# Kernel optimization log

Hardware: AMD Instinct MI355X
Metric: run time of the kernel (lower is better)

The kernel has to match this reference:

```python
import jax, jax.numpy as jnp
from jax import lax
import numpy as np

B = 128   # per-stream batch (hard-coded via torch.zeros(128, ...))
T = 224   # timesteps
L = 224   # per-timestep signal length
H = 12    # LSTM hidden size


def _conv_chain(x, w1, b1, w2, b2):
    # x: [N, 1, 224] -> [N, 1, 28]
    # Conv1d(k=8, s=4, p=2) -> ReLU -> MaxPool1d(k=4, s=2, p=1) -> ReLU -> Conv1d(k=3, s=1, p=1) -> ReLU
    y = lax.conv_general_dilated(x, w1, (4,), [(2, 2)]) + b1[None, :, None]          # [N,1,56]
    y = jax.nn.relu(y)
    y = lax.reduce_window(y, -jnp.inf, lax.max, (1, 1, 4), (1, 1, 2),
                          [(0, 0), (0, 0), (1, 1)])                                   # [N,1,28]
    y = jax.nn.relu(y)
    y = lax.conv_general_dilated(y, w2, (1,), [(1, 1)]) + b2[None, :, None]          # [N,1,28]
    return jax.nn.relu(y)


def _lstm_bidir(x, Wih, Whh, b):
    # x: [B, T, D]; Wih: [2, 4H, D]; Whh: [2, 4H, H]; b: [2, 4H]; gates in PyTorch order i,f,g,o
    Bn, hid = x.shape[0], Whh.shape[-1]

    def run(xs, wih, whh, bb):
        def step(carry, xt):
            h, c = carry
            g = xt @ wih.T + h @ whh.T + bb
            i, f, gg, o = jnp.split(g, 4, axis=-1)
            c = jax.nn.sigmoid(f) * c + jax.nn.sigmoid(i) * jnp.tanh(gg)
            h = jax.nn.sigmoid(o) * jnp.tanh(c)
            return (h, c), h
        h0 = jnp.zeros((Bn, hid), x.dtype)
        _, ys = lax.scan(step, (h0, h0), xs)
        return ys

    xs = jnp.swapaxes(x, 0, 1)                     # [T, B, D]
    fwd = run(xs, Wih[0], Whh[0], b[0])
    bwd = run(xs[::-1], Whh_fix := Wih[1], Whh[1], b[1])[::-1]
    return jnp.swapaxes(jnp.concatenate([fwd, bwd], axis=-1), 0, 1)  # [B, T, 2H]


def _forward(x, c1w1, c1b1, c1w2, c1b2, c2w1, c2b1, c2w2, c2b2,
             l1_0_Wih, l1_0_Whh, l1_0_b, l1_1_Wih, l1_1_Whh, l1_1_b,
             l2_0_Wih, l2_0_Whh, l2_0_b, l2_1_Wih, l2_1_Whh, l2_1_b,
             fcw1, fcb1, fcw2, fcb2, fcw3, fcb3, w1, w2):
    x1 = x[:B, 0]          # [B, 224, 224]
    x2 = x[B:2 * B, 0]     # [B, 224, 224]
    # Fuse the 224-step Python loop: fold time into the batch of the 1D conv.
    y1 = _conv_chain(x1.reshape(B * T, 1, L), c1w1, c1b1, c1w2, c1b2).reshape(B, T, 28)
    y2 = _conv_chain(x2.reshape(B * T, 1, L), c2w1, c2b1, c2w2, c2b2).reshape(B, T, 28)
    o1 = _lstm_bidir(_lstm_bidir(y1, l1_0_Wih, l1_0_Whh, l1_0_b), l1_1_Wih, l1_1_Whh, l1_1_b)
    o2 = _lstm_bidir(_lstm_bidir(y2, l2_0_Wih, l2_0_Whh, l2_0_b), l2_1_Wih, l2_1_Whh, l2_1_b)
    out = w1 * o1 + w2 * o2                       # [B, T, 24]
    out = out.reshape(B, T * 2 * H)               # [B, 5376]
    out = out @ fcw1.T + fcb1                     # [B, 1024]
    out = out @ fcw2.T + fcb2                     # [B, 192]
    return out @ fcw3.T + fcb3                    # [B, 9]


def setup_inputs():
    key = jax.random.key(0)
    ks = iter(jax.random.split(key, 48))

    def rn(shape, scale=0.1):
        return (scale * jax.random.normal(next(ks), shape)).astype(jnp.float32)

    inp = {"x": rn((2 * B, 1, T, L), 1.0)}
    for s in ("c1", "c2"):
        inp[s + "w1"] = rn((1, 1, 8))
        inp[s + "b1"] = rn((1,))
        inp[s + "w2"] = rn((1, 1, 3))
        inp[s + "b2"] = rn((1,))
    for s in ("l1", "l2"):
        for layer, din in ((0, 28), (1, 2 * H)):
            inp[f"{s}_{layer}_Wih"] = rn((2, 4 * H, din))
            inp[f"{s}_{layer}_Whh"] = rn((2, 4 * H, H))
            inp[f"{s}_{layer}_b"] = rn((2, 4 * H))
    inp["fcw1"] = rn((1024, T * 2 * H), 0.02)
    inp["fcb1"] = rn((1024,))
    inp["fcw2"] = rn((192, 1024), 0.05)
    inp["fcb2"] = rn((192,))
    inp["fcw3"] = rn((9, 192), 0.05)
    inp["fcb3"] = rn((9,))
    inp["w1"] = jnp.ones((1,), jnp.float32)
    inp["w2"] = jnp.ones((1,), jnp.float32)
    return inp


def reference(x, c1w1, c1b1, c1w2, c1b2, c2w1, c2b1, c2w2, c2b2,
              l1_0_Wih, l1_0_Whh, l1_0_b, l1_1_Wih, l1_1_Whh, l1_1_b,
              l2_0_Wih, l2_0_Whh, l2_0_b, l2_1_Wih, l2_1_Whh, l2_1_b,
              fcw1, fcb1, fcw2, fcb2, fcw3, fcb3, w1, w2):
    return _forward(x, c1w1, c1b1, c1w2, c1b2, c2w1, c2b1, c2w2, c2b2,
                    l1_0_Wih, l1_0_Whh, l1_0_b, l1_1_Wih, l1_1_Whh, l1_1_b,
                    l2_0_Wih, l2_0_Whh, l2_0_b, l2_1_Wih, l2_1_Whh, l2_1_b,
                    fcw1, fcb1, fcw2, fcb2, fcw3, fcb3, w1, w2)
```

## Files before the change

kernel.cpp:

```cpp
#include <hip/hip_runtime.h>

#define BB 128
#define TT 224
#define LL 224

typedef float v2f __attribute__((ext_vector_type(2)));

__device__ __forceinline__ float rcpf(float x){ return __builtin_amdgcn_rcpf(x); }

#if __has_builtin(__builtin_amdgcn_exp2f)
#define EXP2(x) __builtin_amdgcn_exp2f(x)
#else
#define EXP2(x) __expf((x)*0.6931471805599453f)
#endif

template<int N>
__device__ __forceinline__ float rorN(float x){
  int xi = __builtin_bit_cast(int, x);
  xi = __builtin_amdgcn_update_dpp(xi, xi, 0x120 + N, 0xf, 0xf, false);
  return __builtin_bit_cast(float, xi);
}

__device__ __forceinline__ void swap32(float& a, float& b){
  asm volatile("s_nop 1\n\tv_permlane32_swap_b32 %0, %1\n\ts_nop 1"
               : "+v"(a), "+v"(b));
}

__global__ __launch_bounds__(256) void convpre_kernel(const float* __restrict__ x,
    const float* __restrict__ c1w1, const float* __restrict__ c1b1,
    const float* __restrict__ c1w2, const float* __restrict__ c1b2,
    const float* __restrict__ c2w1, const float* __restrict__ c2b1,
    const float* __restrict__ c2w2, const float* __restrict__ c2b2,
    const float* __restrict__ l10Wih, const float* __restrict__ l10b,
    const float* __restrict__ l20Wih, const float* __restrict__ l20b,
    float* __restrict__ pre,
    const float* __restrict__ fcw2, const float* __restrict__ fcw3,
    float* __restrict__ Wtb)
{
  __shared__ float sb[1440];
  int gb  = blockIdx.x;
  int tid = threadIdx.x;

  if (gb < 36){
    int idx = gb*256 + tid;
    int o = idx >> 10, n = idx & 1023;
    float acc = 0.f;
    for (int p=0;p<192;p++) acc += fcw3[o*192+p]*fcw2[(size_t)p*1024+n];
    Wtb[idx] = acc;
    return;
  }

  float* c1s  = sb;
  float* y4   = sb + 912;

  int blk = gb - 36;
  int branch = (blk >= 1792);
  int lblk = blk - branch*1792;
  int b  = lblk / 14;
  int t0 = (lblk - b*14)*16;
  size_t rbase = ((size_t)(branch*128 + b))*224 + t0;
  size_t prow  = (size_t)b*224 + t0;

  const float* w1 = branch ? c2w1 : c1w1;
  const float* w2 = branch ? c2w2 : c1w2;
  float b1  = branch ? c2b1[0] : c1b1[0];
  float b2v = branch ? c2b2[0] : c1b2[0];
  const float* wih = branch ? l20Wih : l10Wih;
  const float* bia = branch ? l20b   : l10b;

  if (tid < 224){
    int row  = tid / 14, quad = tid - row*14;
    int cj0  = quad*4;
    int bx   = 4*cj0 - 4;
    const float* xrow = x + (rbase + row)*224;
    float w1r[8];
    #pragma unroll
    for (int kk=0;kk<8;kk++) w1r[kk]=w1[kk];
    float xr[24];
    #pragma unroll
    for (int q=0;q<6;q++){
      int idx = bx + 4*q;
      if (idx >= 0 && idx <= 220){
        float4 v = *(const float4*)(xrow + idx);
        xr[4*q]=v.x; xr[4*q+1]=v.y; xr[4*q+2]=v.z; xr[4*q+3]=v.w;
      } else {
        #pragma unroll
        for (int e=0;e<4;e++){
          int ii = idx+e;
          xr[4*q+e] = (ii>=0 && ii<224) ? xrow[ii] : 0.f;
        }
      }
    }
    #pragma unroll
    for (int e=0;e<4;e++){
      float s = b1;
      #pragma unroll
      for (int kk=0;kk<8;kk++) s += xr[4*e+2+kk]*w1r[kk];
      c1s[row*57 + cj0 + e] = fmaxf(s, 0.f);
    }
  }
  __syncthreads();

  for (int i = tid; i < 448; i += 256){
    int row = i / 28, j = i - row*28;
    const float* cr = &c1s[row*57];
    float o = b2v;
    #pragma unroll
    for (int pi=0;pi<3;pi++){
      int p = j - 1 + pi;
      float pool = 0.f;
      if (p>=0 && p<28){
        int i0 = 2*p - 1;
        float m = -1e30f;
        #pragma unroll
        for (int q=0;q<4;q++){
          int ii = i0+q;
          if (ii>=0 && ii<56) m = fmaxf(m, cr[ii]);
        }
        pool = fmaxf(m, 0.f);
      }
      o += pool * w2[pi];
    }
    y4[row*32 + j] = fmaxf(o, 0.f);
  }
  __syncthreads();

  if (tid < 192){
    int d   = tid / 96;
    int g96 = tid - d*96;
    int row = g96 % 48;
    int rrg = g96 / 48;
    const float4* wr = (const float4*)(wih + (d*48 + row)*28);
    float4 wv[7];
    #pragma unroll
    for (int q=0;q<7;q++) wv[q] = wr[q];
    float bias = bia[d*48 + row];
    int unit = row % 12, g = row / 12;
    float* prebase = pre + (size_t)(2*branch + d)*(TT*BB*48) + unit*4 + g;
    #pragma unroll
    for (int rq=0; rq<8; rq++){
      int rr = rrg*8 + rq;
      const float4* yv = (const float4*)&y4[rr*32];
      float acc = bias;
      #pragma unroll
      for (int q=0;q<7;q++){
        float4 yq = yv[q];
        acc += yq.x*wv[q].x + yq.y*wv[q].y + yq.z*wv[q].z + yq.w*wv[q].w;
      }
      prebase[(prow + rr)*48] = acc;
    }
  }
}

#define LSTM_STEP(P, SS) { \
  float x1=rorN<1>(hv), x2=rorN<2>(hv), x3=rorN<3>(hv), x4=rorN<4>(hv), \
        x5=rorN<5>(hv), x6=rorN<6>(hv), x7=rorN<7>(hv), x8=rorN<8>(hv), \
        x9=rorN<9>(hv), x10=rorN<10>(hv), x11=rorN<11>(hv), x12=rorN<12>(hv), \
        x13=rorN<13>(hv), x14=rorN<14>(hv), x15=rorN<15>(hv); \
  v2f a0 = (P); \
  a0 += w[0]*(v2f){hv,hv};   a0 += w[1]*(v2f){x1,x1};   a0 += w[2]*(v2f){x2,x2};   a0 += w[3]*(v2f){x3,x3}; \
  v2f a1 = w[4]*(v2f){x4,x4};   a1 += w[5]*(v2f){x5,x5};   a1 += w[6]*(v2f){x6,x6};   a1 += w[7]*(v2f){x7,x7}; \
  v2f a2 = w[8]*(v2f){x8,x8};   a2 += w[9]*(v2f){x9,x9};   a2 += w[10]*(v2f){x10,x10}; a2 += w[11]*(v2f){x11,x11}; \
  v2f a3 = w[12]*(v2f){x12,x12}; a3 += w[13]*(v2f){x13,x13}; a3 += w[14]*(v2f){x14,x14}; a3 += w[15]*(v2f){x15,x15}; \
  v2f gg = (a0+a1)+(a2+a3); \
  v2f m  = gg*kmul; \
  v2f e  = { EXP2(m.x), EXP2(m.y) }; \
  e += (v2f){1.f,1.f}; \
  v2f d  = { rcpf(e.x), rcpf(e.y) }; \
  v2f res = ca*d + cb; \
  float p0 = res.x, p1 = res.x; swap32(p0, p1); \
  float q0 = res.y, q1 = res.y; swap32(q0, q1); \
  cst = fmaf(q0, cst, p0*p1); \
  float et = EXP2(cst*2.885390082f); \
  float dt = rcpf(et+1.f); \
  hv = q1*fmaf(-2.f, dt, 1.f); \
  hbuf[SS] = hv; }

#define FLUSH8 { \
  if (doSt){ \
    _Pragma("unroll") \
    for (int q=0;q<8;q++) outP[q*ostep] = hbuf[q]; \
  } \
  outP += 8*ostep; }

__global__ __launch_bounds__(64) __attribute__((amdgpu_waves_per_eu(1,1)))
void lstm_kernel(const float* __restrict__ pre,
    const float* __restrict__ whhA, const float* __restrict__ whhB,
    float* __restrict__ out,
    const float* __restrict__ fcw1, const float* __restrict__ fcb1,
    const float* __restrict__ Wtb,
    float* __restrict__ wpart, float* __restrict__ BCpart)
{
  __shared__ float wt[576];
  int blk  = blockIdx.x;
  int lane = threadIdx.x;

  if (blk >= 256){
    int xb  = blk - 256;
    int s   = xb / 84;
    int j64 = xb % 84;
    #pragma unroll
    for (int q=0;q<9;q++) wt[q*64+lane] = Wtb[q*1024 + s*64 + lane];
    __syncthreads();
    int j = j64*64 + lane;
    int nbase = s*64;
    float acc[9];
    #pragma unroll
    for (int o=0;o<9;o++) acc[o]=0.f;
    #pragma unroll 4
    for (int n4=0;n4<16;n4++){
      int nb = nbase + n4*4;
      float4 v4;
      v4.x = fcw1[(size_t)(nb  )*5376 + j];
      v4.y = fcw1[(size_t)(nb+1)*5376 + j];
      v4.z = fcw1[(size_t)(nb+2)*5376 + j];
      v4.w = fcw1[(size_t)(nb+3)*5376 + j];
      #pragma unroll
      for (int o=0;o<9;o++){
        float4 w4 = *(const float4*)&wt[o*64 + n4*4];
        acc[o] += v4.x*w4.x + v4.y*w4.y + v4.z*w4.z + v4.w*w4.w;
      }
    }
    #pragma unroll
    for (int o=0;o<9;o++) wpart[((size_t)s*9+o)*5376 + j] = acc[o];
    if (j64 == 0 && lane < 9){
      float bcp = 0.f;
      for (int n=0;n<64;n++) bcp += wt[lane*64+n]*fcb1[nbase+n];
      BCpart[s*9+lane] = bcp;
    }
    return;
  }

  int r    = blk >> 6;
  int br   = r >> 1, dir = r & 1;
  int u    = lane & 15;
  int bh   = (lane >> 4) & 1;
  int rbit = lane >> 5;
  int keff = (u < 12) ? u : 11;
  int b    = (blk & 63)*2 + bh;
  const float* whh = (br ? whhB : whhA) + dir*48*12;

  v2f w[16];
  #pragma unroll
  for (int rr=0; rr<16; rr++){
    int j = (u - rr) & 15;
    bool vld = (j < 12) && (u < 12);
    int uw = (u < 12) ? u : 0;
    int jw = (j < 12) ? j : 0;
    float wa = whh[((rbit?24:0)  + uw)*12 + jw];
    float wb = whh[((rbit?36:12) + uw)*12 + jw];
    w[rr] = (v2f){ vld ? wa : 0.f, vld ? wb : 0.f };
  }
  const v2f kmul = rbit ? (v2f){2.885390082f, -1.442695041f}
                        : (v2f){-1.442695041f, -1.442695041f};
  const v2f ca   = rbit ? (v2f){-2.f, 1.f} : (v2f){1.f, 1.f};
  const v2f cb   = rbit ? (v2f){ 1.f, 0.f} : (v2f){0.f, 0.f};

  const float* preR = pre + (size_t)r*(TT*BB*48) + (size_t)b*(TT*48) + keff*4 + rbit*2;
  const int sstep = dir ? -48 : 48;
  int scb = dir ? 223*48 : 0;

  v2f pcur[8], pnext[8];
  #pragma unroll
  for (int i=0;i<8;i++) pcur[i]  = *(const v2f*)(preR + scb +  i   *sstep);
  #pragma unroll
  for (int i=0;i<8;i++) pnext[i] = *(const v2f*)(preR + scb + (i+8)*sstep);
  int lb = scb + 16*sstep;

  float hv = 0.f, cst = 0.f;
  float hbuf[8];
  const int ostep = dir ? -24 : 24;
  float* outP = out + (size_t)br*(BB*TT*24) + (size_t)b*TT*24 + dir*12 + u
              + (size_t)(dir ? 223 : 0)*24;
  const bool doSt = (rbit==0) && (u < 12);

  for (int c=0;c<14;c++){
    LSTM_STEP(pcur[0],0) LSTM_STEP(pcur[1],1) LSTM_STEP(pcur[2],2) LSTM_STEP(pcur[3],3)
    LSTM_STEP(pcur[4],4) LSTM_STEP(pcur[5],5) LSTM_STEP(pcur[6],6) LSTM_STEP(pcur[7],7)
    FLUSH8
    if (c < 13){
      #pragma unroll
      for (int i=0;i<8;i++) pcur[i] = *(const v2f*)(preR + lb + i*sstep);
      lb += 8*sstep;
    }
    LSTM_STEP(pnext[0],0) LSTM_STEP(pnext[1],1) LSTM_STEP(pnext[2],2) LSTM_STEP(pnext[3],3)
    LSTM_STEP(pnext[4],4) LSTM_STEP(pnext[5],5) LSTM_STEP(pnext[6],6) LSTM_STEP(pnext[7],7)
    FLUSH8
    if (c < 13){
      #pragma unroll
      for (int i=0;i<8;i++) pnext[i] = *(const v2f*)(preR + lb + i*sstep);
      lb += 8*sstep;
    }
  }
}

__global__ __launch_bounds__(256) void pregate2_kernel(
    const float* __restrict__ in,
    const float* __restrict__ wihA, const float* __restrict__ biasA,
    const float* __restrict__ wihB, const float* __restrict__ biasB,
    float* __restrict__ pre,
    const float* __restrict__ wpart, float* __restrict__ Wc,
    const float* __restrict__ fcw3, const float* __restrict__ fcb2,
    const float* __restrict__ fcb3, const float* __restrict__ BCpart,
    float* __restrict__ BC)
{
  const int D = 24;
  __shared__ float sb[48*24 + 48];
  int gb  = blockIdx.x;
  int tid = threadIdx.x;

  if (gb < 189){
    int idx = gb*256 + tid;
    float a = 0.f;
    #pragma unroll
    for (int s=0;s<16;s++) a += wpart[(size_t)s*48384 + idx];
    Wc[idx] = a;
    return;
  }
  if (gb == 189){
    if (tid < 9){
      float acc = fcb3[tid];
      const float* f3 = fcw3 + tid*192;
      for (int p=0;p<192;p++) acc += f3[p]*fcb2[p];
      #pragma unroll
      for (int s=0;s<16;s++) acc += BCpart[s*9+tid];
      BC[tid] = acc;
    }
    return;
  }

  int pgb = gb - 190;
  float* wL = sb;
  float* bL = sb + 48*D;
  int r = pgb / 1344;
  int lin = (pgb % 1344)*256 + tid;
  int br = r>>1, dir = r&1;
  const float* wih  = (br ? wihB  : wihA)  + dir*48*D;
  const float* bias = (br ? biasB : biasA) + dir*48;
  for (int i = tid; i < 48*D; i += 256) wL[i]=wih[i];
  if (tid < 48) bL[tid]=bias[tid];
  __syncthreads();
  int tb = lin/12;  int k = lin - tb*12;
  const float* rowp = in + (size_t)br*688128 + (size_t)tb*D;
  float aI=bL[k], aF=bL[12+k], aG=bL[24+k], aO=bL[36+k];
  const float4* rp4 = (const float4*)rowp;
  #pragma unroll
  for (int d4=0; d4<D/4; d4++){
    float4 xv = rp4[d4];
    float4 wI = *(const float4*)&wL[(0*12+k)*D + d4*4];
    float4 wF = *(const float4*)&wL[(1*12+k)*D + d4*4];
    float4 wG = *(const float4*)&wL[(2*12+k)*D + d4*4];
    float4 wO = *(const float4*)&wL[(3*12+k)*D + d4*4];
    aI += xv.x*wI.x + xv.y*wI.y + xv.z*wI.z + xv.w*wI.w;
    aF += xv.x*wF.x + xv.y*wF.y + xv.z*wF.z + xv.w*wF.w;
    aG += xv.x*wG.x + xv.y*wG.y + xv.z*wG.z + xv.w*wG.w;
    aO += xv.x*wO.x + xv.y*wO.y + xv.z*wO.z + xv.w*wO.w;
  }
  float4* o = (float4*)(pre + (size_t)r*(TT*BB*48) + (size_t)tb*48 + k*4);
  *o = make_float4(aI,aF,aG,aO);
}

__global__ void final_kernel(const float* __restrict__ o1, const float* __restrict__ o2,
    const float* __restrict__ Wc, const float* __restrict__ BC,
    const float* __restrict__ w1p, const float* __restrict__ w2p,
    float* __restrict__ out)
{
  int wid  = blockIdx.x*4 + (threadIdx.x>>6);
  int lane = threadIdx.x & 63;
  if (wid >= 128*9) return;
  int m = wid / 9, o = wid - m*9;
  float w1 = w1p[0], w2 = w2p[0];
  const float* r1 = o1 + (size_t)m*5376;
  const float* r2 = o2 + (size_t)m*5376;
  const float* wc = Wc + (size_t)o*5376;
  float acc = 0.f;
  for (int i=lane;i<5376;i+=64){
    acc += (w1*r1[i] + w2*r2[i]) * wc[i];
  }
  #pragma unroll
  for (int off=32;off;off>>=1) acc += __shfl_down(acc, off);
  if (lane==0) out[m*9+o] = acc + BC[o];
}

extern "C" void kernel_launch(void* const* d_in, const int* in_sizes, int n_in,
                              void* d_out, int out_size, void* d_ws, size_t ws_size,
                              hipStream_t stream) {
  (void)in_sizes; (void)n_in; (void)out_size; (void)ws_size;
  const float* x    = (const float*)d_in[0];
  const float* c1w1 = (const float*)d_in[1];
  const float* c1b1 = (const float*)d_in[2];
  const float* c1w2 = (const float*)d_in[3];
  const float* c1b2 = (const float*)d_in[4];
  const float* c2w1 = (const float*)d_in[5];
  const float* c2b1 = (const float*)d_in[6];
  const float* c2w2 = (const float*)d_in[7];
  const float* c2b2 = (const float*)d_in[8];
  const float* l10Wih = (const float*)d_in[9];
  const float* l10Whh = (const float*)d_in[10];
  const float* l10b   = (const float*)d_in[11];
  const float* l11Wih = (const float*)d_in[12];
  const float* l11Whh = (const float*)d_in[13];
  const float* l11b   = (const float*)d_in[14];
  const float* l20Wih = (const float*)d_in[15];
  const float* l20Whh = (const float*)d_in[16];
  const float* l20b   = (const float*)d_in[17];
  const float* l21Wih = (const float*)d_in[18];
  const float* l21Whh = (const float*)d_in[19];
  const float* l21b   = (const float*)d_in[20];
  const float* fcw1 = (const float*)d_in[21];
  const float* fcb1 = (const float*)d_in[22];
  const float* fcw2 = (const float*)d_in[23];
  const float* fcb2 = (const float*)d_in[24];
  const float* fcw3 = (const float*)d_in[25];
  const float* fcb3 = (const float*)d_in[26];
  const float* w1   = (const float*)d_in[27];
  const float* w2   = (const float*)d_in[28];
  float* out = (float*)d_out;

  float* ws  = (float*)d_ws;
  float* wpart = ws;
  float* pre  = ws  + 2*802816;
  float* ol0  = pre + 4*1376256;
  float* ol1  = ol0 + 2*688128;
  float* Wc   = ol1 + 2*688128;
  float* BC   = Wc  + 48384;
  float* BCpart = BC + 9;
  float* Wtb  = BCpart + 144;

  convpre_kernel<<<3620,256,0,stream>>>(x, c1w1,c1b1,c1w2,c1b2, c2w1,c2b1,c2w2,c2b2,
      l10Wih, l10b, l20Wih, l20b, pre, fcw2, fcw3, Wtb);
  lstm_kernel<<<1600,64,0,stream>>>(pre, l10Whh, l20Whh, ol0,
      fcw1, fcb1, Wtb, wpart, BCpart);
  pregate2_kernel<<<5566,256,0,stream>>>(ol0, l11Wih, l11b, l21Wih, l21b, pre, wpart, Wc,
      fcw3, fcb2, fcb3, BCpart, BC);
  lstm_kernel<<<256,64,0,stream>>>(pre, l11Whh, l21Whh, ol1,
      fcw1, fcb1, Wtb, wpart, BCpart);
  final_kernel<<<288,256,0,stream>>>(ol1, ol1+688128, Wc, BC, w1, w2, out);
}
```

Measured before the change: 163.0 us.

## Move Wc/BC reduction into second LSTM launch and enlarge conv tiles

The Wc partial-sum reduction and BC bias computation move out of pregate2_kernel into spare blocks of the second lstm_kernel launch, selected by a phase flag. They now run alongside the latency-bound recurrent blocks, which otherwise leave the GPU mostly idle, and pregate2 sheds 190 blocks. convpre_kernel also handles 32 timesteps per block instead of 16, with 8 conv outputs per thread, halving the block count and amortizing weight loads at the cost of more shared memory and registers.

```diff
diff --git a/kernel.cpp b/kernel.cpp
--- a/kernel.cpp
+++ b/kernel.cpp
@@ -37,7 +37,7 @@
     const float* __restrict__ fcw2, const float* __restrict__ fcw3,
     float* __restrict__ Wtb)
 {
-  __shared__ float sb[1440];
+  __shared__ float sb[2848];
   int gb  = blockIdx.x;
   int tid = threadIdx.x;
 
@@ -51,13 +51,13 @@
   }
 
   float* c1s  = sb;
-  float* y4   = sb + 912;
+  float* y4   = sb + 1824;
 
   int blk = gb - 36;
-  int branch = (blk >= 1792);
-  int lblk = blk - branch*1792;
-  int b  = lblk / 14;
-  int t0 = (lblk - b*14)*16;
+  int branch = (blk >= 896);
+  int lblk = blk - branch*896;
+  int b  = lblk / 7;
+  int t0 = (lblk - b*7)*32;
   size_t rbase = ((size_t)(branch*128 + b))*224 + t0;
   size_t prow  = (size_t)b*224 + t0;
 
@@ -69,16 +69,16 @@
   const float* bia = branch ? l20b   : l10b;
 
   if (tid < 224){
-    int row  = tid / 14, quad = tid - row*14;
-    int cj0  = quad*4;
+    int row  = tid / 7, grp = tid - row*7;
+    int cj0  = grp*8;
     int bx   = 4*cj0 - 4;
     const float* xrow = x + (rbase + row)*224;
     float w1r[8];
     #pragma unroll
     for (int kk=0;kk<8;kk++) w1r[kk]=w1[kk];
-    float xr[24];
-    #pragma unroll
-    for (int q=0;q<6;q++){
+    float xr[40];
+    #pragma unroll
+    for (int q=0;q<10;q++){
       int idx = bx + 4*q;
       if (idx >= 0 && idx <= 220){
         float4 v = *(const float4*)(xrow + idx);
@@ -92,7 +92,7 @@
       }
     }
     #pragma unroll
-    for (int e=0;e<4;e++){
+    for (int e=0;e<8;e++){
       float s = b1;
       #pragma unroll
       for (int kk=0;kk<8;kk++) s += xr[4*e+2+kk]*w1r[kk];
@@ -101,7 +101,7 @@
   }
   __syncthreads();
 
-  for (int i = tid; i < 448; i += 256){
+  for (int i = tid; i < 896; i += 256){
     int row = i / 28, j = i - row*28;
     const float* cr = &c1s[row*57];
     float o = b2v;
@@ -138,8 +138,8 @@
     int unit = row % 12, g = row / 12;
     float* prebase = pre + (size_t)(2*branch + d)*(TT*BB*48) + unit*4 + g;
     #pragma unroll
-    for (int rq=0; rq<8; rq++){
-      int rr = rrg*8 + rq;
+    for (int rq=0; rq<16; rq++){
+      int rr = rrg*16 + rq;
       const float4* yv = (const float4*)&y4[rr*32];
       float acc = bias;
       #pragma unroll
@@ -189,7 +189,10 @@
     float* __restrict__ out,
     const float* __restrict__ fcw1, const float* __restrict__ fcb1,
     const float* __restrict__ Wtb,
-    float* __restrict__ wpart, float* __restrict__ BCpart)
+    float* __restrict__ wpart, float* __restrict__ BCpart,
+    const float* __restrict__ fcw3, const float* __restrict__ fcb2,
+    const float* __restrict__ fcb3, float* __restrict__ Wc,
+    float* __restrict__ BC, int phase)
 {
   __shared__ float wt[576];
   int blk  = blockIdx.x;
@@ -197,36 +200,56 @@
 
   if (blk >= 256){
     int xb  = blk - 256;
-    int s   = xb / 84;
-    int j64 = xb % 84;
-    #pragma unroll
-    for (int q=0;q<9;q++) wt[q*64+lane] = Wtb[q*1024 + s*64 + lane];
-    __syncthreads();
-    int j = j64*64 + lane;
-    int nbase = s*64;
-    float acc[9];
-    #pragma unroll
-    for (int o=0;o<9;o++) acc[o]=0.f;
-    #pragma unroll 4
-    for (int n4=0;n4<16;n4++){
-      int nb = nbase + n4*4;
-      float4 v4;
-      v4.x = fcw1[(size_t)(nb  )*5376 + j];
-      v4.y = fcw1[(size_t)(nb+1)*5376 + j];
-      v4.z = fcw1[(size_t)(nb+2)*5376 + j];
-      v4.w = fcw1[(size_t)(nb+3)*5376 + j];
-      #pragma unroll
-      for (int o=0;o<9;o++){
-        float4 w4 = *(const float4*)&wt[o*64 + n4*4];
-        acc[o] += v4.x*w4.x + v4.y*w4.y + v4.z*w4.z + v4.w*w4.w;
-      }
-    }
-    #pragma unroll
-    for (int o=0;o<9;o++) wpart[((size_t)s*9+o)*5376 + j] = acc[o];
-    if (j64 == 0 && lane < 9){
-      float bcp = 0.f;
-      for (int n=0;n<64;n++) bcp += wt[lane*64+n]*fcb1[nbase+n];
-      BCpart[s*9+lane] = bcp;
+    if (phase == 0){
+      int s   = xb / 84;
+      int j64 = xb % 84;
+      #pragma unroll
+      for (int q=0;q<9;q++) wt[q*64+lane] = Wtb[q*1024 + s*64 + lane];
+      __syncthreads();
+      int j = j64*64 + lane;
+      int nbase = s*64;
+      float acc[9];
+      #pragma unroll
+      for (int o=0;o<9;o++) acc[o]=0.f;
+      #pragma unroll 4
+      for (int n4=0;n4<16;n4++){
+        int nb = nbase + n4*4;
+        float4 v4;
+        v4.x = fcw1[(size_t)(nb  )*5376 + j];
+        v4.y = fcw1[(size_t)(nb+1)*5376 + j];
+        v4.z = fcw1[(size_t)(nb+2)*5376 + j];
+        v4.w = fcw1[(size_t)(nb+3)*5376 + j];
+        #pragma unroll
+        for (int o=0;o<9;o++){
+          float4 w4 = *(const float4*)&wt[o*64 + n4*4];
+          acc[o] += v4.x*w4.x + v4.y*w4.y + v4.z*w4.z + v4.w*w4.w;
+        }
+      }
+      #pragma unroll
+      for (int o=0;o<9;o++) wpart[((size_t)s*9+o)*5376 + j] = acc[o];
+      if (j64 == 0 && lane < 9){
+        float bcp = 0.f;
+        for (int n=0;n<64;n++) bcp += wt[lane*64+n]*fcb1[nbase+n];
+        BCpart[s*9+lane] = bcp;
+      }
+    } else {
+      if (xb < 189){
+        #pragma unroll
+        for (int q=0;q<4;q++){
+          int idx = xb*256 + q*64 + lane;
+          float a = 0.f;
+          #pragma unroll
+          for (int s=0;s<16;s++) a += wpart[(size_t)s*48384 + idx];
+          Wc[idx] = a;
+        }
+      } else if (lane < 9){
+        float acc = fcb3[lane];
+        const float* f3 = fcw3 + lane*192;
+        for (int p=0;p<192;p++) acc += f3[p]*fcb2[p];
+        #pragma unroll
+        for (int s=0;s<16;s++) acc += BCpart[s*9+lane];
+        BC[lane] = acc;
+      }
     }
     return;
   }
@@ -298,42 +321,17 @@
     const float* __restrict__ in,
     const float* __restrict__ wihA, const float* __restrict__ biasA,
     const float* __restrict__ wihB, const float* __restrict__ biasB,
-    float* __restrict__ pre,
-    const float* __restrict__ wpart, float* __restrict__ Wc,
-    const float* __restrict__ fcw3, const float* __restrict__ fcb2,
-    const float* __restrict__ fcb3, const float* __restrict__ BCpart,
-    float* __restrict__ BC)
+    float* __restrict__ pre)
 {
   const int D = 24;
   __shared__ float sb[48*24 + 48];
   int gb  = blockIdx.x;
   int tid = threadIdx.x;
 
-  if (gb < 189){
-    int idx = gb*256 + tid;
-    float a = 0.f;
-    #pragma unroll
-    for (int s=0;s<16;s++) a += wpart[(size_t)s*48384 + idx];
-    Wc[idx] = a;
-    return;
-  }
-  if (gb == 189){
-    if (tid < 9){
-      float acc = fcb3[tid];
-      const float* f3 = fcw3 + tid*192;
-      for (int p=0;p<192;p++) acc += f3[p]*fcb2[p];
-      #pragma unroll
-      for (int s=0;s<16;s++) acc += BCpart[s*9+tid];
-      BC[tid] = acc;
-    }
-    return;
-  }
-
-  int pgb = gb - 190;
   float* wL = sb;
   float* bL = sb + 48*D;
-  int r = pgb / 1344;
-  int lin = (pgb % 1344)*256 + tid;
+  int r = gb / 1344;
+  int lin = (gb % 1344)*256 + tid;
   int br = r>>1, dir = r&1;
   const float* wih  = (br ? wihB  : wihA)  + dir*48*D;
   const float* bias = (br ? biasB : biasA) + dir*48;
@@ -427,13 +425,12 @@
   float* BCpart = BC + 9;
   float* Wtb  = BCpart + 144;
 
-  convpre_kernel<<<3620,256,0,stream>>>(x, c1w1,c1b1,c1w2,c1b2, c2w1,c2b1,c2w2,c2b2,
+  convpre_kernel<<<1828,256,0,stream>>>(x, c1w1,c1b1,c1w2,c1b2, c2w1,c2b1,c2w2,c2b2,
       l10Wih, l10b, l20Wih, l20b, pre, fcw2, fcw3, Wtb);
   lstm_kernel<<<1600,64,0,stream>>>(pre, l10Whh, l20Whh, ol0,
-      fcw1, fcb1, Wtb, wpart, BCpart);
-  pregate2_kernel<<<5566,256,0,stream>>>(ol0, l11Wih, l11b, l21Wih, l21b, pre, wpart, Wc,
-      fcw3, fcb2, fcb3, BCpart, BC);
-  lstm_kernel<<<256,64,0,stream>>>(pre, l11Whh, l21Whh, ol1,
-      fcw1, fcb1, Wtb, wpart, BCpart);
+      fcw1, fcb1, Wtb, wpart, BCpart, fcw3, fcb2, fcb3, Wc, BC, 0);
+  pregate2_kernel<<<5376,256,0,stream>>>(ol0, l11Wih, l11b, l21Wih, l21b, pre);
+  lstm_kernel<<<446,64,0,stream>>>(pre, l11Whh, l21Whh, ol1,
+      fcw1, fcb1, Wtb, wpart, BCpart, fcw3, fcb2, fcb3, Wc, BC, 1);
   final_kernel<<<288,256,0,stream>>>(ol1, ol1+688128, Wc, BC, w1, w2, out);
 }
```

New measurement: 202.0 us. 1.24x slower.

## Fuse layer-2 input projection into LSTM kernel with producer-consumer waves

Applied to the files above, without the earlier changes.

Replaces the separate pregate2 kernel, which wrote layer-2 input gate preactivations to global memory, with a fused kernel. In it, three producer waves compute the Wih·x projection into shared memory while one consumer wave runs the recurrence, synchronised through volatile progress counters and spin-waits. The goal is to drop the global round trip of the pre buffer and overlap the projection with the serial recurrence. The costs are large shared-memory use per block, limited occupancy, and spin-wait overhead. The Wc/BC reduction moves to its own small kernel.

```diff
diff --git a/kernel.cpp b/kernel.cpp
--- a/kernel.cpp
+++ b/kernel.cpp
@@ -294,70 +294,154 @@
   }
 }
 
-__global__ __launch_bounds__(256) void pregate2_kernel(
-    const float* __restrict__ in,
+__global__ __launch_bounds__(256) __attribute__((amdgpu_waves_per_eu(1,1)))
+void lstm2_fused_kernel(const float* __restrict__ ol0,
+    const float* __restrict__ whhA, const float* __restrict__ whhB,
     const float* __restrict__ wihA, const float* __restrict__ biasA,
     const float* __restrict__ wihB, const float* __restrict__ biasB,
-    float* __restrict__ pre,
+    float* __restrict__ out)
+{
+  __shared__ float lpre[2*224*48];
+  __shared__ int prog[4];
+  int tid  = threadIdx.x;
+  int blk  = blockIdx.x;
+  int r    = blk >> 6;
+  int br   = r >> 1, dir = r & 1;
+  int b0   = (blk & 63)*2;
+
+  if (tid < 4) ((volatile int*)prog)[tid] = 0;
+  __syncthreads();
+
+  if (tid >= 64){
+    int p    = tid - 64;
+    int wv   = p >> 6;
+    int e    = p % 96;
+    int th   = p / 96;
+    int bb   = e / 48;
+    int gate = e % 48;
+    const float* wih2 = (br ? wihB : wihA) + (dir*48 + gate)*24;
+    float4 wq[6];
+    #pragma unroll
+    for (int q=0;q<6;q++) wq[q] = ((const float4*)wih2)[q];
+    float bias = (br ? biasB : biasA)[dir*48 + gate];
+    int unit = gate % 12, gg = gate / 12;
+    const float* olrow = ol0 + (size_t)br*(BB*TT*24) + (size_t)(b0+bb)*TT*24;
+    float* lrow = lpre + bb*(224*48) + unit*4 + gg;
+    volatile int* pv = prog;
+
+    for (int g=0; g<28; g++){
+      #pragma unroll
+      for (int si=0; si<4; si++){
+        int step = g*8 + th*4 + si;
+        int t = dir ? 223 - step : step;
+        const float4* xr = (const float4*)(olrow + t*24);
+        float a = bias;
+        #pragma unroll
+        for (int q=0;q<6;q++){
+          float4 xq = xr[q];
+          a += xq.x*wq[q].x + xq.y*wq[q].y + xq.z*wq[q].z + xq.w*wq[q].w;
+        }
+        lrow[t*48] = a;
+      }
+      asm volatile("s_waitcnt lgkmcnt(0) vmcnt(0)" ::: "memory");
+      if ((p & 63) == 0) pv[wv] = g+1;
+    }
+    return;
+  }
+
+  int lane = tid;
+  int u    = lane & 15;
+  int bh   = (lane >> 4) & 1;
+  int rbit = lane >> 5;
+  int keff = (u < 12) ? u : 11;
+  int b    = b0 + bh;
+  const float* whh = (br ? whhB : whhA) + dir*48*12;
+
+  v2f w[16];
+  #pragma unroll
+  for (int rr=0; rr<16; rr++){
+    int j = (u - rr) & 15;
+    bool vld = (j < 12) && (u < 12);
+    int uw = (u < 12) ? u : 0;
+    int jw = (j < 12) ? j : 0;
+    float wa = whh[((rbit?24:0)  + uw)*12 + jw];
+    float wb = whh[((rbit?36:12) + uw)*12 + jw];
+    w[rr] = (v2f){ vld ? wa : 0.f, vld ? wb : 0.f };
+  }
+  const v2f kmul = rbit ? (v2f){2.885390082f, -1.442695041f}
+                        : (v2f){-1.442695041f, -1.442695041f};
+  const v2f ca   = rbit ? (v2f){-2.f, 1.f} : (v2f){1.f, 1.f};
+  const v2f cb   = rbit ? (v2f){ 1.f, 0.f} : (v2f){0.f, 0.f};
+
+  float* preR = lpre + bh*(224*48) + keff*4 + rbit*2;
+  const int sstep = dir ? -48 : 48;
+  int scb = dir ? 223*48 : 0;
+  volatile int* pv = prog;
+
+#define WAITG(NEED) { int nd_ = (NEED); \
+  while (pv[0] < nd_ || pv[1] < nd_ || pv[2] < nd_) __builtin_amdgcn_s_sleep(2); \
+  asm volatile("" ::: "memory"); }
+
+  WAITG(2)
+  v2f pcur[8], pnext[8];
+  #pragma unroll
+  for (int i=0;i<8;i++) pcur[i]  = *(const v2f*)(preR + scb +  i   *sstep);
+  #pragma unroll
+  for (int i=0;i<8;i++) pnext[i] = *(const v2f*)(preR + scb + (i+8)*sstep);
+  int lb = scb + 16*sstep;
+
+  float hv = 0.f, cst = 0.f;
+  float hbuf[8];
+  const int ostep = dir ? -24 : 24;
+  float* outP = out + (size_t)br*(BB*TT*24) + (size_t)b*TT*24 + dir*12 + u
+              + (size_t)(dir ? 223 : 0)*24;
+  const bool doSt = (rbit==0) && (u < 12);
+
+  for (int c=0;c<14;c++){
+    LSTM_STEP(pcur[0],0) LSTM_STEP(pcur[1],1) LSTM_STEP(pcur[2],2) LSTM_STEP(pcur[3],3)
+    LSTM_STEP(pcur[4],4) LSTM_STEP(pcur[5],5) LSTM_STEP(pcur[6],6) LSTM_STEP(pcur[7],7)
+    FLUSH8
+    if (c < 13){
+      WAITG(2*c+3)
+      #pragma unroll
+      for (int i=0;i<8;i++) pcur[i] = *(const v2f*)(preR + lb + i*sstep);
+      lb += 8*sstep;
+    }
+    LSTM_STEP(pnext[0],0) LSTM_STEP(pnext[1],1) LSTM_STEP(pnext[2],2) LSTM_STEP(pnext[3],3)
+    LSTM_STEP(pnext[4],4) LSTM_STEP(pnext[5],5) LSTM_STEP(pnext[6],6) LSTM_STEP(pnext[7],7)
+    FLUSH8
+    if (c < 13){
+      WAITG(2*c+4)
+      #pragma unroll
+      for (int i=0;i<8;i++) pnext[i] = *(const v2f*)(preR + lb + i*sstep);
+      lb += 8*sstep;
+    }
+  }
+#undef WAITG
+}
+
+__global__ __launch_bounds__(256) void wpartB_kernel(
     const float* __restrict__ wpart, float* __restrict__ Wc,
     const float* __restrict__ fcw3, const float* __restrict__ fcb2,
     const float* __restrict__ fcb3, const float* __restrict__ BCpart,
     float* __restrict__ BC)
 {
-  const int D = 24;
-  __shared__ float sb[48*24 + 48];
   int gb  = blockIdx.x;
   int tid = threadIdx.x;
-
   if (gb < 189){
     int idx = gb*256 + tid;
     float a = 0.f;
     #pragma unroll
     for (int s=0;s<16;s++) a += wpart[(size_t)s*48384 + idx];
     Wc[idx] = a;
-    return;
-  }
-  if (gb == 189){
-    if (tid < 9){
-      float acc = fcb3[tid];
-      const float* f3 = fcw3 + tid*192;
-      for (int p=0;p<192;p++) acc += f3[p]*fcb2[p];
-      #pragma unroll
-      for (int s=0;s<16;s++) acc += BCpart[s*9+tid];
-      BC[tid] = acc;
-    }
-    return;
-  }
-
-  int pgb = gb - 190;
-  float* wL = sb;
-  float* bL = sb + 48*D;
-  int r = pgb / 1344;
-  int lin = (pgb % 1344)*256 + tid;
-  int br = r>>1, dir = r&1;
-  const float* wih  = (br ? wihB  : wihA)  + dir*48*D;
-  const float* bias = (br ? biasB : biasA) + dir*48;
-  for (int i = tid; i < 48*D; i += 256) wL[i]=wih[i];
-  if (tid < 48) bL[tid]=bias[tid];
-  __syncthreads();
-  int tb = lin/12;  int k = lin - tb*12;
-  const float* rowp = in + (size_t)br*688128 + (size_t)tb*D;
-  float aI=bL[k], aF=bL[12+k], aG=bL[24+k], aO=bL[36+k];
-  const float4* rp4 = (const float4*)rowp;
-  #pragma unroll
-  for (int d4=0; d4<D/4; d4++){
-    float4 xv = rp4[d4];
-    float4 wI = *(const float4*)&wL[(0*12+k)*D + d4*4];
-    float4 wF = *(const float4*)&wL[(1*12+k)*D + d4*4];
-    float4 wG = *(const float4*)&wL[(2*12+k)*D + d4*4];
-    float4 wO = *(const float4*)&wL[(3*12+k)*D + d4*4];
-    aI += xv.x*wI.x + xv.y*wI.y + xv.z*wI.z + xv.w*wI.w;
-    aF += xv.x*wF.x + xv.y*wF.y + xv.z*wF.z + xv.w*wF.w;
-    aG += xv.x*wG.x + xv.y*wG.y + xv.z*wG.z + xv.w*wG.w;
-    aO += xv.x*wO.x + xv.y*wO.y + xv.z*wO.z + xv.w*wO.w;
-  }
-  float4* o = (float4*)(pre + (size_t)r*(TT*BB*48) + (size_t)tb*48 + k*4);
-  *o = make_float4(aI,aF,aG,aO);
+  } else if (tid < 9){
+    float acc = fcb3[tid];
+    const float* f3 = fcw3 + tid*192;
+    for (int p=0;p<192;p++) acc += f3[p]*fcb2[p];
+    #pragma unroll
+    for (int s=0;s<16;s++) acc += BCpart[s*9+tid];
+    BC[tid] = acc;
+  }
 }
 
 __global__ void final_kernel(const float* __restrict__ o1, const float* __restrict__ o2,
@@ -431,9 +515,8 @@
       l10Wih, l10b, l20Wih, l20b, pre, fcw2, fcw3, Wtb);
   lstm_kernel<<<1600,64,0,stream>>>(pre, l10Whh, l20Whh, ol0,
       fcw1, fcb1, Wtb, wpart, BCpart);
-  pregate2_kernel<<<5566,256,0,stream>>>(ol0, l11Wih, l11b, l21Wih, l21b, pre, wpart, Wc,
-      fcw3, fcb2, fcb3, BCpart, BC);
-  lstm_kernel<<<256,64,0,stream>>>(pre, l11Whh, l21Whh, ol1,
-      fcw1, fcb1, Wtb, wpart, BCpart);
+  wpartB_kernel<<<190,256,0,stream>>>(wpart, Wc, fcw3, fcb2, fcb3, BCpart, BC);
+  lstm2_fused_kernel<<<256,256,0,stream>>>(ol0, l11Whh, l21Whh,
+      l11Wih, l11b, l21Wih, l21b, ol1);
   final_kernel<<<288,256,0,stream>>>(ol1, ol1+688128, Wc, BC, w1, w2, out);
 }
```

After: 158.5 us. -2.8%, faster.
